# Optimization experiments

Measured on AMD Instinct MI355X. Metric: run time of the kernel, lower is better.

## Reference

```python
import jax, jax.numpy as jnp
import numpy as np

N = 50000      # nodes
E = 200000     # edges
IN = 768       # in_dim
HID = 256      # hidden_dim
OUT = 64       # out_dim
H = 4          # heads in conv1
R = 6          # n_relations
NEG = 0.2      # LeakyReLU negative slope (PyG default)
EPS = 1e-5     # LayerNorm eps


def layer_norm(h, g, b):
    mu = jnp.mean(h, axis=-1, keepdims=True)
    var = jnp.mean((h - mu) ** 2, axis=-1, keepdims=True)
    return (h - mu) * jax.lax.rsqrt(var + EPS) * g + b


def gat_layer(x, src, dst, W, a_src, a_dst, bias, heads, dh):
    # project: [N, heads, dh]
    h = (x @ W).reshape(-1, heads, dh)
    # per-node attention logits [N, heads]
    al_s = jnp.sum(h * a_src, axis=-1)
    al_d = jnp.sum(h * a_dst, axis=-1)
    # per-edge scores (edge j->i: source contributes al_s[j], target al_d[i])
    e = jax.nn.leaky_relu(al_s[src] + al_d[dst], NEG)  # [E, heads]
    # segment softmax over edges sharing the same destination node
    e_max = jax.ops.segment_max(e, dst, num_segments=N)        # [N, heads]
    ex = jnp.exp(e - e_max[dst])                               # [E, heads]
    denom = jax.ops.segment_sum(ex, dst, num_segments=N)       # [N, heads]
    alpha = ex / denom[dst]                                    # [E, heads]
    # weighted scatter-aggregate of source messages
    msg = h[src] * alpha[:, :, None]                            # [E, heads, dh]
    out = jax.ops.segment_sum(msg, dst, num_segments=N)        # [N, heads, dh]
    return out.reshape(-1, heads * dh) + bias


def setup_inputs() -> dict:
    key = jax.random.key(0)
    ks = jax.random.split(key, 16)
    s = 0.05  # keep attention logits tame
    return {
        "x": jax.random.normal(ks[0], (N, IN), jnp.float32),
        "edge_index": jax.random.randint(ks[1], (2, E), 0, N, dtype=jnp.int64),
        "edge_type": jax.random.randint(ks[2], (E,), 0, R, dtype=jnp.int64),
        "edge_emb": jax.random.normal(ks[3], (R, IN), jnp.float32) * s,
        "W1": jax.random.normal(ks[4], (IN, H * (HID // H)), jnp.float32) * s,
        "a_src1": jax.random.normal(ks[5], (H, HID // H), jnp.float32) * s,
        "a_dst1": jax.random.normal(ks[6], (H, HID // H), jnp.float32) * s,
        "b1": jnp.zeros((HID,), jnp.float32),
        "g1": jnp.ones((HID,), jnp.float32),
        "be1": jnp.zeros((HID,), jnp.float32),
        "W2": jax.random.normal(ks[7], (HID, OUT), jnp.float32) * s,
        "a_src2": jax.random.normal(ks[8], (1, OUT), jnp.float32) * s,
        "a_dst2": jax.random.normal(ks[9], (1, OUT), jnp.float32) * s,
        "b2": jnp.zeros((OUT,), jnp.float32),
        "g2": jnp.ones((OUT,), jnp.float32),
        "be2": jnp.zeros((OUT,), jnp.float32),
    }


def reference(x, edge_index, edge_type, edge_emb, W1, a_src1, a_dst1, b1, g1, be1,
              W2, a_src2, a_dst2, b2, g2, be2):
    src, dst = edge_index[0], edge_index[1]
    edge_feat = edge_emb[edge_type]                 # [E, IN]
    x_mod = x.at[src].set(x[src] + edge_feat)
    h = gat_layer(x_mod, src, dst, W1, a_src1, a_dst1, b1, H, HID // H)
    h = layer_norm(h, g1, be1)
    h = jax.nn.elu(h)                                # dropout off (inference)
    h = gat_layer(h, src, dst, W2, a_src2, a_dst2, b2, 1, OUT)
    h = layer_norm(h, g2, be2)
    return h
```

## Files before the change

kernel.cpp:

```cpp
#include <hip/hip_runtime.h>
#include <cstdint>
#include <cstddef>

#define NN 50000
#define NE 200000
#define IND 768
#define HID 256
#define OUTD 64
#define NB 196
#define NEB 782
#define NWB 1024
#define NCB 2048

typedef __bf16 bf16;
typedef __bf16 bf16x8 __attribute__((ext_vector_type(8)));
typedef __bf16 bf16x4 __attribute__((ext_vector_type(4)));
typedef float f32x4 __attribute__((ext_vector_type(4)));

__global__ __launch_bounds__(256) void k_front(const int* __restrict__ ei,
                                               int* __restrict__ le, int* __restrict__ deg,
                                               const float* __restrict__ x,
                                               bf16* __restrict__ A1,
                                               const float* __restrict__ W1,
                                               const float* __restrict__ W2,
                                               const float* __restrict__ eemb,
                                               bf16* __restrict__ W1t,
                                               bf16* __restrict__ W2t,
                                               float* __restrict__ eW) {
  const int bid = blockIdx.x, tid = threadIdx.x;
  if (bid < NWB) {
    int bx = bid >> 8, by = bid & 255;
    if (bx < 3) {
      int k = bx * 256 + tid;
      W1t[by * IND + k] = (bf16)W1[(size_t)k * HID + by];
    } else if (by < OUTD) {
      W2t[by * HID + tid] = (bf16)W2[(size_t)tid * OUTD + by];
    } else if (by < OUTD + 7) {
      int r = by - OUTD;
      float s0 = 0.f, s1 = 0.f, s2 = 0.f, s3 = 0.f;
      if (r < 6) {
        const float* er = eemb + (size_t)r * IND;
#pragma unroll 4
        for (int k = 0; k < IND; k += 4) {
          s0 += er[k]     * W1[(size_t)k * HID + tid];
          s1 += er[k + 1] * W1[(size_t)(k + 1) * HID + tid];
          s2 += er[k + 2] * W1[(size_t)(k + 2) * HID + tid];
          s3 += er[k + 3] * W1[(size_t)(k + 3) * HID + tid];
        }
      }
      eW[r * HID + tid] = (s0 + s1) + (s2 + s3);
    }
  } else if (bid < NWB + NCB) {
    const size_t total = (size_t)NN * IND / 8;
    const int cb = bid - NWB;
    for (size_t idx = (size_t)cb * 256 + tid; idx < total; idx += (size_t)NCB * 256) {
      const float* px = x + idx * 8;
      float4 v0 = *(const float4*)px, v1 = *(const float4*)(px + 4);
      bf16x8 o;
      o[0] = (bf16)v0.x; o[1] = (bf16)v0.y; o[2] = (bf16)v0.z; o[3] = (bf16)v0.w;
      o[4] = (bf16)v1.x; o[5] = (bf16)v1.y; o[6] = (bf16)v1.z; o[7] = (bf16)v1.w;
      *(bf16x8*)(A1 + idx * 8) = o;
    }
  } else {
    int e = (bid - NWB - NCB) * 256 + tid;
    if (e < NE) {
      atomicMax(&le[ei[e]], e);
      atomicAdd(&deg[ei[NE + e]], 1);
    }
  }
}

__global__ __launch_bounds__(256) void k_scan_block(const int* __restrict__ deg,
                                                    int* __restrict__ excl, int* __restrict__ bsum) {
  __shared__ int sm[256];
  int tid = threadIdx.x;
  int i = blockIdx.x * 256 + tid;
  int v = (i < NN) ? deg[i] : 0;
  sm[tid] = v;
  __syncthreads();
#pragma unroll
  for (int off = 1; off < 256; off <<= 1) {
    int t = (tid >= off) ? sm[tid - off] : 0;
    __syncthreads();
    sm[tid] += t;
    __syncthreads();
  }
  if (i < NN) excl[i] = sm[tid] - v;
  if (tid == 255) bsum[blockIdx.x] = sm[255];
}

__global__ __launch_bounds__(256) void k_scan_partials(const int* __restrict__ bsum,
                                                       int* __restrict__ bbase) {
  __shared__ int sm[256];
  int tid = threadIdx.x;
  int v = (tid < NB) ? bsum[tid] : 0;
  sm[tid] = v;
  __syncthreads();
#pragma unroll
  for (int off = 1; off < 256; off <<= 1) {
    int t = (tid >= off) ? sm[tid - off] : 0;
    __syncthreads();
    sm[tid] += t;
    __syncthreads();
  }
  bbase[tid] = sm[tid] - v;
}

__global__ __launch_bounds__(256) void k_add_base(const int* __restrict__ excl,
                                                  const int* __restrict__ bbase,
                                                  int* __restrict__ rowstart, int* __restrict__ cur,
                                                  const int* __restrict__ le,
                                                  const int* __restrict__ et,
                                                  int* __restrict__ eidx) {
  int i = blockIdx.x * 256 + threadIdx.x;
  if (i < NN) {
    int rs = excl[i] + bbase[i >> 8];
    rowstart[i] = rs;
    cur[i] = rs;
    int l = le[i];
    eidx[i] = (l >= 0) ? et[l] : 6;
  }
}

__global__ __launch_bounds__(256) void k_scatter_csr(const int* __restrict__ ei,
                                                     int* __restrict__ cur, int* __restrict__ csr) {
  int e = blockIdx.x * 256 + threadIdx.x;
  if (e < NE) {
    int d = ei[NE + e];
    int pos = atomicAdd(&cur[d], 1);
    csr[pos] = ei[e];
  }
}

__device__ __forceinline__ void gld16(const bf16* g, bf16* l) {
  __builtin_amdgcn_global_load_lds((const __attribute__((address_space(1))) void*)g,
                                   (__attribute__((address_space(3))) void*)l, 16, 0, 0);
}

template <typename OutT, int TN, bool EW>
__global__ __launch_bounds__(256) void k_gemm_bt(const bf16* __restrict__ A,
                                                 const bf16* __restrict__ Bt,
                                                 OutT* __restrict__ C,
                                                 int M, int K, int NC,
                                                 const float* __restrict__ aS,
                                                 const float* __restrict__ aD,
                                                 float* __restrict__ alS,
                                                 float* __restrict__ alD,
                                                 int alStride,
                                                 const int* __restrict__ eidx,
                                                 const float* __restrict__ eW) {
  constexpr int MI = (TN == 128) ? 4 : 2;
  constexpr int WROWS = MI * 16;
  __shared__ bf16 As[3][128 * 32];
  __shared__ bf16 Bs[3][TN * 32];
  const int tid = threadIdx.x;
  const int lane = tid & 63;
  const int wave = tid >> 6;
  const int wr = (TN == 128) ? (wave >> 1) : wave;
  const int wc = (TN == 128) ? (wave & 1) : 0;
  const int ln15 = lane & 15, q = lane >> 4;
  const int n0 = blockIdx.x * TN;
  const int m0 = blockIdx.y * 128;

  const int sr = lane >> 2;
  const int scol = (lane & 3) * 8;
  const int gA0 = min(m0 + wave * 32 + sr, M - 1);
  const int gA1 = min(m0 + wave * 32 + 16 + sr, M - 1);
  int gB0, gB1 = 0;
  if constexpr (TN == 128) {
    gB0 = min(n0 + wave * 32 + sr, NC - 1);
    gB1 = min(n0 + wave * 32 + 16 + sr, NC - 1);
  } else {
    gB0 = min(n0 + wave * 16 + sr, NC - 1);
  }

  auto stage = [&](int buf, int kt) {
    gld16(A + (size_t)gA0 * K + kt + scol, &As[buf][(wave * 32) * 32]);
    gld16(A + (size_t)gA1 * K + kt + scol, &As[buf][(wave * 32 + 16) * 32]);
    if constexpr (TN == 128) {
      gld16(Bt + (size_t)gB0 * K + kt + scol, &Bs[buf][(wave * 32) * 32]);
      gld16(Bt + (size_t)gB1 * K + kt + scol, &Bs[buf][(wave * 32 + 16) * 32]);
    } else {
      gld16(Bt + (size_t)gB0 * K + kt + scol, &Bs[buf][(wave * 16) * 32]);
    }
  };

  f32x4 acc[MI][4] = {};

  auto compute = [&](int buf) {
    bf16x8 af[MI], bfr[4];
#pragma unroll
    for (int i = 0; i < MI; i++)
      af[i] = *(const bf16x8*)(&As[buf][(wr * WROWS + i * 16 + ln15) * 32 + q * 8]);
#pragma unroll
    for (int i = 0; i < 4; i++)
      bfr[i] = *(const bf16x8*)(&Bs[buf][(wc * 64 + i * 16 + ln15) * 32 + q * 8]);
#pragma unroll
    for (int mi = 0; mi < MI; mi++)
#pragma unroll
      for (int ni = 0; ni < 4; ni++)
        acc[mi][ni] = __builtin_amdgcn_mfma_f32_16x16x32_bf16(af[mi], bfr[ni], acc[mi][ni], 0, 0, 0);
  };

  const int NT = K >> 5;

  stage(0, 0);
  stage(1, 32);
  for (int t = 0; t < NT; ++t) {
    if (t + 2 < NT) {
      if constexpr (TN == 128) asm volatile("s_waitcnt vmcnt(4)" ::: "memory");
      else                     asm volatile("s_waitcnt vmcnt(3)" ::: "memory");
    } else {
      asm volatile("s_waitcnt vmcnt(0)" ::: "memory");
    }
    __builtin_amdgcn_sched_barrier(0);
    __builtin_amdgcn_s_barrier();
    if (t + 2 < NT) stage((t + 2) % 3, (t + 2) << 5);
    compute(t % 3);
    asm volatile("s_waitcnt lgkmcnt(0)" ::: "memory");
    __builtin_amdgcn_sched_barrier(0);
  }

  if constexpr (EW) {
#pragma unroll
    for (int mi = 0; mi < MI; mi++)
#pragma unroll
      for (int r = 0; r < 4; r++) {
        int row = m0 + wr * WROWS + mi * 16 + q * 4 + r;
        int e = eidx[min(row, M - 1)];
        const float* ew = eW + e * HID + n0 + wc * 64 + ln15;
#pragma unroll
        for (int ni = 0; ni < 4; ni++) acc[mi][ni][r] += ew[ni * 16];
      }
  }

#pragma unroll
  for (int mi = 0; mi < MI; mi++)
#pragma unroll
    for (int ni = 0; ni < 4; ni++)
#pragma unroll
      for (int r = 0; r < 4; r++) {
        int row = m0 + wr * WROWS + mi * 16 + q * 4 + r;
        int col = n0 + wc * 64 + ni * 16 + ln15;
        if (row < M && col < NC) C[(size_t)row * NC + col] = (OutT)acc[mi][ni][r];
      }

  if (n0 + wc * 64 < NC) {
    const int hd = (n0 + wc * 64) >> 6;
#pragma unroll
    for (int mi = 0; mi < MI; mi++)
#pragma unroll
      for (int r = 0; r < 4; r++) {
        float ps = 0.f, pd = 0.f;
#pragma unroll
        for (int ni = 0; ni < 4; ni++) {
          int col = n0 + wc * 64 + ni * 16 + ln15;
          float w_s = (col < NC) ? aS[col] : 0.f;
          float w_d = (col < NC) ? aD[col] : 0.f;
          ps += acc[mi][ni][r] * w_s;
          pd += acc[mi][ni][r] * w_d;
        }
#pragma unroll
        for (int off = 1; off < 16; off <<= 1) {
          ps += __shfl_xor(ps, off);
          pd += __shfl_xor(pd, off);
        }
        int row = m0 + wr * WROWS + mi * 16 + q * 4 + r;
        if (ln15 == 0 && row < M) {
          alS[row * alStride + hd] = ps;
          alD[row * alStride + hd] = pd;
        }
      }
  }
}

__global__ __launch_bounds__(256) void k_agg_ln1(const int* __restrict__ rowstart,
                                                 const int* __restrict__ deg,
                                                 const int* __restrict__ csr,
                                                 const bf16* __restrict__ h1,
                                                 const float* __restrict__ alS,
                                                 const float* __restrict__ alD,
                                                 const float* __restrict__ b1,
                                                 const float* __restrict__ g1,
                                                 const float* __restrict__ be1,
                                                 bf16* __restrict__ hln) {
  const int n = blockIdx.x * 4 + (threadIdx.x >> 6);
  const int lane = threadIdx.x & 63;
  const int f0 = lane * 4;
  const int hd = lane >> 4;
  int start = rowstart[n], cnt = deg[n];
  float ald = alD[n * 4 + hd];
  float accv0 = 0.f, accv1 = 0.f, accv2 = 0.f, accv3 = 0.f, accw = 0.f;
  for (int j = 0; j < cnt; j++) {
    int s = csr[start + j];
    float logit = alS[s * 4 + hd] + ald;
    logit = logit >= 0.f ? logit : 0.2f * logit;
    float w = __expf(logit);
    bf16x4 hv = *(const bf16x4*)(h1 + (size_t)s * HID + f0);
    accv0 += w * (float)hv[0];
    accv1 += w * (float)hv[1];
    accv2 += w * (float)hv[2];
    accv3 += w * (float)hv[3];
    accw += w;
  }
  float inv = (cnt > 0) ? 1.f / accw : 0.f;
  float4 bv = *(const float4*)(b1 + f0);
  float v0 = accv0 * inv + bv.x;
  float v1 = accv1 * inv + bv.y;
  float v2 = accv2 * inv + bv.z;
  float v3 = accv3 * inv + bv.w;
  float s = v0 + v1 + v2 + v3;
  float ss = v0 * v0 + v1 * v1 + v2 * v2 + v3 * v3;
#pragma unroll
  for (int off = 32; off; off >>= 1) { s += __shfl_xor(s, off); ss += __shfl_xor(ss, off); }
  float mu = s * (1.f / HID);
  float var = ss * (1.f / HID) - mu * mu;
  float rs = rsqrtf(var + 1e-5f);
  float4 gv = *(const float4*)(g1 + f0);
  float4 ev = *(const float4*)(be1 + f0);
  float y0 = (v0 - mu) * rs * gv.x + ev.x;
  float y1 = (v1 - mu) * rs * gv.y + ev.y;
  float y2 = (v2 - mu) * rs * gv.z + ev.z;
  float y3 = (v3 - mu) * rs * gv.w + ev.w;
  y0 = y0 > 0.f ? y0 : __expf(y0) - 1.f;
  y1 = y1 > 0.f ? y1 : __expf(y1) - 1.f;
  y2 = y2 > 0.f ? y2 : __expf(y2) - 1.f;
  y3 = y3 > 0.f ? y3 : __expf(y3) - 1.f;
  bf16x4 o;
  o[0] = (bf16)y0; o[1] = (bf16)y1; o[2] = (bf16)y2; o[3] = (bf16)y3;
  *(bf16x4*)(hln + (size_t)n * HID + f0) = o;
}

__global__ __launch_bounds__(256) void k_agg_ln2(const int* __restrict__ rowstart,
                                                 const int* __restrict__ deg,
                                                 const int* __restrict__ csr,
                                                 const float* __restrict__ h2,
                                                 const float* __restrict__ alS,
                                                 const float* __restrict__ alD,
                                                 const float* __restrict__ b2,
                                                 const float* __restrict__ g2,
                                                 const float* __restrict__ be2,
                                                 float* __restrict__ out) {
  const int n = blockIdx.x * 4 + (threadIdx.x >> 6);
  const int f = threadIdx.x & 63;
  int start = rowstart[n], cnt = deg[n];
  float ald = alD[n];
  float accv = 0.f, accw = 0.f;
  for (int j = 0; j < cnt; j++) {
    int s = csr[start + j];
    float logit = alS[s] + ald;
    logit = logit >= 0.f ? logit : 0.2f * logit;
    float w = __expf(logit);
    accv += w * h2[(size_t)s * OUTD + f];
    accw += w;
  }
  float v = (cnt > 0) ? accv / accw : 0.f;
  v += b2[f];
  float s = v, ss = v * v;
#pragma unroll
  for (int off = 32; off; off >>= 1) { s += __shfl_xor(s, off); ss += __shfl_xor(ss, off); }
  float mu = s * (1.f / OUTD);
  float var = ss * (1.f / OUTD) - mu * mu;
  out[(size_t)n * OUTD + f] = (v - mu) * rsqrtf(var + 1e-5f) * g2[f] + be2[f];
}

extern "C" void kernel_launch(void* const* d_in, const int* in_sizes, int n_in,
                              void* d_out, int out_size, void* d_ws, size_t ws_size,
                              hipStream_t stream) {
  const float* x    = (const float*)d_in[0];
  const int*   ei   = (const int*)d_in[1];
  const int*   et   = (const int*)d_in[2];
  const float* eemb = (const float*)d_in[3];
  const float* W1   = (const float*)d_in[4];
  const float* as1  = (const float*)d_in[5];
  const float* ad1  = (const float*)d_in[6];
  const float* b1   = (const float*)d_in[7];
  const float* g1   = (const float*)d_in[8];
  const float* be1  = (const float*)d_in[9];
  const float* W2   = (const float*)d_in[10];
  const float* as2  = (const float*)d_in[11];
  const float* ad2  = (const float*)d_in[12];
  const float* b2   = (const float*)d_in[13];
  const float* g2   = (const float*)d_in[14];
  const float* be2  = (const float*)d_in[15];
  float* out = (float*)d_out;

  char* base = (char*)d_ws;
  size_t off = 0;
  auto alloc = [&](size_t bytes) -> void* {
    void* p = base + off;
    off = (off + bytes + 255) & ~(size_t)255;
    return p;
  };
  int*   le    = (int*)alloc((size_t)NN * 4);
  int*   deg   = (int*)alloc((size_t)NN * 4);
  int*   excl  = (int*)alloc((size_t)NN * 4);
  int*   bsum  = (int*)alloc(256 * 4);
  int*   bbase = (int*)alloc(256 * 4);
  int*   rowst = (int*)alloc((size_t)NN * 4);
  int*   cur   = (int*)alloc((size_t)NN * 4);
  int*   eidx  = (int*)alloc((size_t)NN * 4);
  int*   csr   = (int*)alloc((size_t)NE * 4);
  bf16*  h1    = (bf16*)alloc((size_t)NN * HID * 2);
  float* alS1  = (float*)alloc((size_t)NN * 4 * 4);
  float* alD1  = (float*)alloc((size_t)NN * 4 * 4);
  bf16*  W1t   = (bf16*)alloc((size_t)HID * IND * 2);
  bf16*  W2t   = (bf16*)alloc((size_t)OUTD * HID * 2);
  float* eW    = (float*)alloc((size_t)7 * HID * 4);
  char*  R     = (char*)alloc((size_t)NN * IND * 2);
  bf16*  A1    = (bf16*)R;
  bf16*  hln   = (bf16*)R;
  float* h2    = (float*)(R + (size_t)NN * HID * 2);
  float* alS2  = (float*)(R + (size_t)NN * HID * 2 + (size_t)NN * OUTD * 4);
  float* alD2  = (float*)(R + (size_t)NN * HID * 2 + (size_t)NN * OUTD * 4 + (size_t)NN * 4);

  hipMemsetAsync(le, 0xFF, (size_t)NN * 4, stream);
  hipMemsetAsync(deg, 0, (size_t)NN * 4, stream);

  k_front<<<NWB + NCB + NEB, 256, 0, stream>>>(ei, le, deg, x, A1, W1, W2, eemb, W1t, W2t, eW);
  k_scan_block<<<NB, 256, 0, stream>>>(deg, excl, bsum);
  k_scan_partials<<<1, 256, 0, stream>>>(bsum, bbase);
  k_add_base<<<NB, 256, 0, stream>>>(excl, bbase, rowst, cur, le, et, eidx);
  k_scatter_csr<<<NEB, 256, 0, stream>>>(ei, cur, csr);

  k_gemm_bt<bf16, 128, true><<<dim3(2, (NN + 127) / 128), 256, 0, stream>>>(
      A1, W1t, h1, NN, IND, HID, as1, ad1, alS1, alD1, 4, eidx, eW);
  k_agg_ln1<<<NN / 4, 256, 0, stream>>>(rowst, deg, csr, h1, alS1, alD1, b1, g1, be1, hln);

  k_gemm_bt<float, 64, false><<<dim3(1, (NN + 127) / 128), 256, 0, stream>>>(
      hln, W2t, h2, NN, HID, OUTD, as2, ad2, alS2, alD2, 1, nullptr, nullptr);
  k_agg_ln2<<<NN / 4, 256, 0, stream>>>(rowst, deg, csr, h2, alS2, alD2, b2, g2, be2, out);
}
```

Before: 437.4 us.

## Widen layer-1 GEMM tile to full 256 columns and reorder front blocks

The layer-1 projection GEMM becomes a dedicated 512-thread kernel whose 128x256 tile covers all output columns. Each A row tile is now loaded once instead of once per column half, which halves A-operand global traffic, at the cost of more LDS per block and possibly lower occupancy. The layer-2 GEMM is specialised into its own kernel with the compile-time constants fixed. The fused front kernel now puts the edge atomic blocks first so they are scheduled early, ahead of the large bf16 conversion work.

```diff
diff --git a/kernel.cpp b/kernel.cpp
--- a/kernel.cpp
+++ b/kernel.cpp
@@ -28,8 +28,14 @@
                                                bf16* __restrict__ W2t,
                                                float* __restrict__ eW) {
   const int bid = blockIdx.x, tid = threadIdx.x;
-  if (bid < NWB) {
-    int bx = bid >> 8, by = bid & 255;
+  if (bid < NEB) {
+    int e = bid * 256 + tid;
+    if (e < NE) {
+      atomicMax(&le[ei[e]], e);
+      atomicAdd(&deg[ei[NE + e]], 1);
+    }
+  } else if (bid < NEB + NWB) {
+    int wb = bid - NEB, bx = wb >> 8, by = wb & 255;
     if (bx < 3) {
       int k = bx * 256 + tid;
       W1t[by * IND + k] = (bf16)W1[(size_t)k * HID + by];
@@ -50,9 +56,9 @@
       }
       eW[r * HID + tid] = (s0 + s1) + (s2 + s3);
     }
-  } else if (bid < NWB + NCB) {
+  } else {
     const size_t total = (size_t)NN * IND / 8;
-    const int cb = bid - NWB;
+    const int cb = bid - NEB - NWB;
     for (size_t idx = (size_t)cb * 256 + tid; idx < total; idx += (size_t)NCB * 256) {
       const float* px = x + idx * 8;
       float4 v0 = *(const float4*)px, v1 = *(const float4*)(px + 4);
@@ -60,12 +66,6 @@
       o[0] = (bf16)v0.x; o[1] = (bf16)v0.y; o[2] = (bf16)v0.z; o[3] = (bf16)v0.w;
       o[4] = (bf16)v1.x; o[5] = (bf16)v1.y; o[6] = (bf16)v1.z; o[7] = (bf16)v1.w;
       *(bf16x8*)(A1 + idx * 8) = o;
-    }
-  } else {
-    int e = (bid - NWB - NCB) * 256 + tid;
-    if (e < NE) {
-      atomicMax(&le[ei[e]], e);
-      atomicAdd(&deg[ei[NE + e]], 1);
     }
   }
 }
@@ -137,66 +137,50 @@
                                    (__attribute__((address_space(3))) void*)l, 16, 0, 0);
 }
 
-template <typename OutT, int TN, bool EW>
-__global__ __launch_bounds__(256) void k_gemm_bt(const bf16* __restrict__ A,
-                                                 const bf16* __restrict__ Bt,
-                                                 OutT* __restrict__ C,
-                                                 int M, int K, int NC,
-                                                 const float* __restrict__ aS,
-                                                 const float* __restrict__ aD,
-                                                 float* __restrict__ alS,
-                                                 float* __restrict__ alD,
-                                                 int alStride,
-                                                 const int* __restrict__ eidx,
-                                                 const float* __restrict__ eW) {
-  constexpr int MI = (TN == 128) ? 4 : 2;
-  constexpr int WROWS = MI * 16;
+__global__ __launch_bounds__(512) void k_gemm1(const bf16* __restrict__ A,
+                                               const bf16* __restrict__ Bt,
+                                               bf16* __restrict__ C,
+                                               const float* __restrict__ aS,
+                                               const float* __restrict__ aD,
+                                               float* __restrict__ alS,
+                                               float* __restrict__ alD,
+                                               const int* __restrict__ eidx,
+                                               const float* __restrict__ eW) {
+  const int M = NN, K = IND;
   __shared__ bf16 As[3][128 * 32];
-  __shared__ bf16 Bs[3][TN * 32];
+  __shared__ bf16 Bs[3][256 * 32];
   const int tid = threadIdx.x;
   const int lane = tid & 63;
   const int wave = tid >> 6;
-  const int wr = (TN == 128) ? (wave >> 1) : wave;
-  const int wc = (TN == 128) ? (wave & 1) : 0;
+  const int wr = wave >> 2;
+  const int wc = wave & 3;
   const int ln15 = lane & 15, q = lane >> 4;
-  const int n0 = blockIdx.x * TN;
-  const int m0 = blockIdx.y * 128;
+  const int m0 = blockIdx.x * 128;
 
   const int sr = lane >> 2;
   const int scol = (lane & 3) * 8;
-  const int gA0 = min(m0 + wave * 32 + sr, M - 1);
-  const int gA1 = min(m0 + wave * 32 + 16 + sr, M - 1);
-  int gB0, gB1 = 0;
-  if constexpr (TN == 128) {
-    gB0 = min(n0 + wave * 32 + sr, NC - 1);
-    gB1 = min(n0 + wave * 32 + 16 + sr, NC - 1);
-  } else {
-    gB0 = min(n0 + wave * 16 + sr, NC - 1);
-  }
+  const int gA0 = min(m0 + wave * 16 + sr, M - 1);
+  const int gB0 = wave * 32 + sr;
+  const int gB1 = wave * 32 + 16 + sr;
 
   auto stage = [&](int buf, int kt) {
-    gld16(A + (size_t)gA0 * K + kt + scol, &As[buf][(wave * 32) * 32]);
-    gld16(A + (size_t)gA1 * K + kt + scol, &As[buf][(wave * 32 + 16) * 32]);
-    if constexpr (TN == 128) {
-      gld16(Bt + (size_t)gB0 * K + kt + scol, &Bs[buf][(wave * 32) * 32]);
-      gld16(Bt + (size_t)gB1 * K + kt + scol, &Bs[buf][(wave * 32 + 16) * 32]);
-    } else {
-      gld16(Bt + (size_t)gB0 * K + kt + scol, &Bs[buf][(wave * 16) * 32]);
-    }
+    gld16(A + (size_t)gA0 * K + kt + scol, &As[buf][(wave * 16) * 32]);
+    gld16(Bt + (size_t)gB0 * K + kt + scol, &Bs[buf][(wave * 32) * 32]);
+    gld16(Bt + (size_t)gB1 * K + kt + scol, &Bs[buf][(wave * 32 + 16) * 32]);
   };
 
-  f32x4 acc[MI][4] = {};
+  f32x4 acc[4][4] = {};
 
   auto compute = [&](int buf) {
-    bf16x8 af[MI], bfr[4];
-#pragma unroll
-    for (int i = 0; i < MI; i++)
-      af[i] = *(const bf16x8*)(&As[buf][(wr * WROWS + i * 16 + ln15) * 32 + q * 8]);
+    bf16x8 af[4], bfr[4];
+#pragma unroll
+    for (int i = 0; i < 4; i++)
+      af[i] = *(const bf16x8*)(&As[buf][(wr * 64 + i * 16 + ln15) * 32 + q * 8]);
 #pragma unroll
     for (int i = 0; i < 4; i++)
       bfr[i] = *(const bf16x8*)(&Bs[buf][(wc * 64 + i * 16 + ln15) * 32 + q * 8]);
 #pragma unroll
-    for (int mi = 0; mi < MI; mi++)
+    for (int mi = 0; mi < 4; mi++)
 #pragma unroll
       for (int ni = 0; ni < 4; ni++)
         acc[mi][ni] = __builtin_amdgcn_mfma_f32_16x16x32_bf16(af[mi], bfr[ni], acc[mi][ni], 0, 0, 0);
@@ -207,12 +191,8 @@
   stage(0, 0);
   stage(1, 32);
   for (int t = 0; t < NT; ++t) {
-    if (t + 2 < NT) {
-      if constexpr (TN == 128) asm volatile("s_waitcnt vmcnt(4)" ::: "memory");
-      else                     asm volatile("s_waitcnt vmcnt(3)" ::: "memory");
-    } else {
-      asm volatile("s_waitcnt vmcnt(0)" ::: "memory");
-    }
+    if (t + 2 < NT) asm volatile("s_waitcnt vmcnt(3)" ::: "memory");
+    else            asm volatile("s_waitcnt vmcnt(0)" ::: "memory");
     __builtin_amdgcn_sched_barrier(0);
     __builtin_amdgcn_s_barrier();
     if (t + 2 < NT) stage((t + 2) % 3, (t + 2) << 5);
@@ -221,57 +201,148 @@
     __builtin_amdgcn_sched_barrier(0);
   }
 
-  if constexpr (EW) {
-#pragma unroll
-    for (int mi = 0; mi < MI; mi++)
+#pragma unroll
+  for (int mi = 0; mi < 4; mi++)
+#pragma unroll
+    for (int r = 0; r < 4; r++) {
+      int row = m0 + wr * 64 + mi * 16 + q * 4 + r;
+      int e = eidx[min(row, M - 1)];
+      const float* ew = eW + e * HID + wc * 64 + ln15;
+#pragma unroll
+      for (int ni = 0; ni < 4; ni++) acc[mi][ni][r] += ew[ni * 16];
+    }
+
+#pragma unroll
+  for (int mi = 0; mi < 4; mi++)
+#pragma unroll
+    for (int ni = 0; ni < 4; ni++)
 #pragma unroll
       for (int r = 0; r < 4; r++) {
-        int row = m0 + wr * WROWS + mi * 16 + q * 4 + r;
-        int e = eidx[min(row, M - 1)];
-        const float* ew = eW + e * HID + n0 + wc * 64 + ln15;
-#pragma unroll
-        for (int ni = 0; ni < 4; ni++) acc[mi][ni][r] += ew[ni * 16];
-      }
-  }
-
-#pragma unroll
-  for (int mi = 0; mi < MI; mi++)
-#pragma unroll
-    for (int ni = 0; ni < 4; ni++)
-#pragma unroll
-      for (int r = 0; r < 4; r++) {
-        int row = m0 + wr * WROWS + mi * 16 + q * 4 + r;
-        int col = n0 + wc * 64 + ni * 16 + ln15;
-        if (row < M && col < NC) C[(size_t)row * NC + col] = (OutT)acc[mi][ni][r];
-      }
-
-  if (n0 + wc * 64 < NC) {
-    const int hd = (n0 + wc * 64) >> 6;
-#pragma unroll
-    for (int mi = 0; mi < MI; mi++)
+        int row = m0 + wr * 64 + mi * 16 + q * 4 + r;
+        int col = wc * 64 + ni * 16 + ln15;
+        if (row < M) C[(size_t)row * HID + col] = (bf16)acc[mi][ni][r];
+      }
+
+  {
+    const int hd = wc;
+#pragma unroll
+    for (int mi = 0; mi < 4; mi++)
 #pragma unroll
       for (int r = 0; r < 4; r++) {
         float ps = 0.f, pd = 0.f;
 #pragma unroll
         for (int ni = 0; ni < 4; ni++) {
-          int col = n0 + wc * 64 + ni * 16 + ln15;
-          float w_s = (col < NC) ? aS[col] : 0.f;
-          float w_d = (col < NC) ? aD[col] : 0.f;
-          ps += acc[mi][ni][r] * w_s;
-          pd += acc[mi][ni][r] * w_d;
+          int col = wc * 64 + ni * 16 + ln15;
+          ps += acc[mi][ni][r] * aS[col];
+          pd += acc[mi][ni][r] * aD[col];
         }
 #pragma unroll
         for (int off = 1; off < 16; off <<= 1) {
           ps += __shfl_xor(ps, off);
           pd += __shfl_xor(pd, off);
         }
-        int row = m0 + wr * WROWS + mi * 16 + q * 4 + r;
+        int row = m0 + wr * 64 + mi * 16 + q * 4 + r;
         if (ln15 == 0 && row < M) {
-          alS[row * alStride + hd] = ps;
-          alD[row * alStride + hd] = pd;
+          alS[row * 4 + hd] = ps;
+          alD[row * 4 + hd] = pd;
         }
       }
   }
+}
+
+__global__ __launch_bounds__(256) void k_gemm2(const bf16* __restrict__ A,
+                                               const bf16* __restrict__ Bt,
+                                               float* __restrict__ C,
+                                               const float* __restrict__ aS,
+                                               const float* __restrict__ aD,
+                                               float* __restrict__ alS,
+                                               float* __restrict__ alD) {
+  const int M = NN, K = HID, NC = OUTD;
+  __shared__ bf16 As[3][128 * 32];
+  __shared__ bf16 Bs[3][64 * 32];
+  const int tid = threadIdx.x;
+  const int lane = tid & 63;
+  const int wave = tid >> 6;
+  const int ln15 = lane & 15, q = lane >> 4;
+  const int m0 = blockIdx.x * 128;
+
+  const int sr = lane >> 2;
+  const int scol = (lane & 3) * 8;
+  const int gA0 = min(m0 + wave * 32 + sr, M - 1);
+  const int gA1 = min(m0 + wave * 32 + 16 + sr, M - 1);
+  const int gB0 = min(wave * 16 + sr, NC - 1);
+
+  auto stage = [&](int buf, int kt) {
+    gld16(A + (size_t)gA0 * K + kt + scol, &As[buf][(wave * 32) * 32]);
+    gld16(A + (size_t)gA1 * K + kt + scol, &As[buf][(wave * 32 + 16) * 32]);
+    gld16(Bt + (size_t)gB0 * K + kt + scol, &Bs[buf][(wave * 16) * 32]);
+  };
+
+  f32x4 acc[2][4] = {};
+
+  auto compute = [&](int buf) {
+    bf16x8 af[2], bfr[4];
+#pragma unroll
+    for (int i = 0; i < 2; i++)
+      af[i] = *(const bf16x8*)(&As[buf][(wave * 32 + i * 16 + ln15) * 32 + q * 8]);
+#pragma unroll
+    for (int i = 0; i < 4; i++)
+      bfr[i] = *(const bf16x8*)(&Bs[buf][(i * 16 + ln15) * 32 + q * 8]);
+#pragma unroll
+    for (int mi = 0; mi < 2; mi++)
+#pragma unroll
+      for (int ni = 0; ni < 4; ni++)
+        acc[mi][ni] = __builtin_amdgcn_mfma_f32_16x16x32_bf16(af[mi], bfr[ni], acc[mi][ni], 0, 0, 0);
+  };
+
+  const int NT = K >> 5;
+
+  stage(0, 0);
+  stage(1, 32);
+  for (int t = 0; t < NT; ++t) {
+    if (t + 2 < NT) asm volatile("s_waitcnt vmcnt(3)" ::: "memory");
+    else            asm volatile("s_waitcnt vmcnt(0)" ::: "memory");
+    __builtin_amdgcn_sched_barrier(0);
+    __builtin_amdgcn_s_barrier();
+    if (t + 2 < NT) stage((t + 2) % 3, (t + 2) << 5);
+    compute(t % 3);
+    asm volatile("s_waitcnt lgkmcnt(0)" ::: "memory");
+    __builtin_amdgcn_sched_barrier(0);
+  }
+
+#pragma unroll
+  for (int mi = 0; mi < 2; mi++)
+#pragma unroll
+    for (int ni = 0; ni < 4; ni++)
+#pragma unroll
+      for (int r = 0; r < 4; r++) {
+        int row = m0 + wave * 32 + mi * 16 + q * 4 + r;
+        int col = ni * 16 + ln15;
+        if (row < M) C[(size_t)row * NC + col] = acc[mi][ni][r];
+      }
+
+#pragma unroll
+  for (int mi = 0; mi < 2; mi++)
+#pragma unroll
+    for (int r = 0; r < 4; r++) {
+      float ps = 0.f, pd = 0.f;
+#pragma unroll
+      for (int ni = 0; ni < 4; ni++) {
+        int col = ni * 16 + ln15;
+        ps += acc[mi][ni][r] * aS[col];
+        pd += acc[mi][ni][r] * aD[col];
+      }
+#pragma unroll
+      for (int off = 1; off < 16; off <<= 1) {
+        ps += __shfl_xor(ps, off);
+        pd += __shfl_xor(pd, off);
+      }
+      int row = m0 + wave * 32 + mi * 16 + q * 4 + r;
+      if (ln15 == 0 && row < M) {
+        alS[row] = ps;
+        alD[row] = pd;
+      }
+    }
 }
 
 __global__ __launch_bounds__(256) void k_agg_ln1(const int* __restrict__ rowstart,
@@ -417,17 +488,15 @@
   hipMemsetAsync(le, 0xFF, (size_t)NN * 4, stream);
   hipMemsetAsync(deg, 0, (size_t)NN * 4, stream);
 
-  k_front<<<NWB + NCB + NEB, 256, 0, stream>>>(ei, le, deg, x, A1, W1, W2, eemb, W1t, W2t, eW);
+  k_front<<<NEB + NWB + NCB, 256, 0, stream>>>(ei, le, deg, x, A1, W1, W2, eemb, W1t, W2t, eW);
   k_scan_block<<<NB, 256, 0, stream>>>(deg, excl, bsum);
   k_scan_partials<<<1, 256, 0, stream>>>(bsum, bbase);
   k_add_base<<<NB, 256, 0, stream>>>(excl, bbase, rowst, cur, le, et, eidx);
   k_scatter_csr<<<NEB, 256, 0, stream>>>(ei, cur, csr);
 
-  k_gemm_bt<bf16, 128, true><<<dim3(2, (NN + 127) / 128), 256, 0, stream>>>(
-      A1, W1t, h1, NN, IND, HID, as1, ad1, alS1, alD1, 4, eidx, eW);
+  k_gemm1<<<(NN + 127) / 128, 512, 0, stream>>>(A1, W1t, h1, as1, ad1, alS1, alD1, eidx, eW);
   k_agg_ln1<<<NN / 4, 256, 0, stream>>>(rowst, deg, csr, h1, alS1, alD1, b1, g1, be1, hln);
 
-  k_gemm_bt<float, 64, false><<<dim3(1, (NN + 127) / 128), 256, 0, stream>>>(
-      hln, W2t, h2, NN, HID, OUTD, as2, ad2, alS2, alD2, 1, nullptr, nullptr);
+  k_gemm2<<<(NN + 127) / 128, 256, 0, stream>>>(hln, W2t, h2, as2, ad2, alS2, alD2);
   k_agg_ln2<<<NN / 4, 256, 0, stream>>>(rowst, deg, csr, h2, alS2, alD2, b2, g2, be2, out);
 }
```

New measurement: 445.9 us. Within noise of the previous version (+1.9%).
